# Kernel optimization log

Measured on AMD Instinct MI355X. Metric: run time of the kernel, lower is better.

The kernel has to match this reference:

```python
import jax, jax.numpy as jnp
import numpy as np

B, L, C, S, W, R = 2, 32, 32, 64, 64, 32
MH = 32  # forcing MLP hidden


def _conv3d(x, w, b, pad_hw):
    # x: [B, Cin, L, S, W], w: [Cout, Cin, 1, kh, kw]
    y = jax.lax.conv_general_dilated(
        x, w, window_strides=(1, 1, 1),
        padding=[(0, 0), (pad_hw, pad_hw), (pad_hw, pad_hw)],
        dimension_numbers=('NCDHW', 'OIDHW', 'NCDHW'))
    return y + b[None, :, None, None, None]


def _forward(x, listT, params_log_base, dispersion_mod, fm_W1, fm_b1, fm_W2, fm_b2,
             forcing_scale, U_re, U_im, V_re, V_im, pW_re, pW_im, pb_re, pb_im,
             convr_w, convr_b, convi_w, convi_b, projc_w, projc_b, ln_w, ln_b):
    b, l, c, s, w = x.shape
    r = U_re.shape[-1]
    pad = s // 4
    dt = listT.reshape(b, l, 1, 1, 1)

    # FFT with mirror padding along S
    xp = jnp.pad(x, ((0, 0), (0, 0), (0, 0), (pad, pad), (0, 0)), mode='reflect')
    h = jnp.fft.fft2(xp.astype(jnp.complex64), axes=(-2, -1), norm='ortho')

    # complex channel projection
    proj_W = pW_re + 1j * pW_im
    h = jnp.einsum('blcsw,cd->bldsw', h, proj_W)
    h = h + (pb_re + 1j * pb_im)[None, None, :, None, None]

    # back to spatial, crop pad, re-FFT
    hs = jnp.fft.ifft2(h, axes=(-2, -1), norm='ortho')[..., pad:-pad, :]
    h = jnp.fft.fft2(hs, axes=(-2, -1), norm='ortho')

    U = U_re + 1j * U_im          # [C, S, R]
    V = V_re + 1j * V_im          # [C, W, R]
    # zq[b,l,c,r,q] = sum_{s,w} h * conj(U)[c,s,r] * V[c,w,q]
    zq = jnp.einsum('blcsw,csr,cwq->blcrq', h, jnp.conj(U), V)

    nu_base = jnp.exp(params_log_base[0] + dispersion_mod[0]).reshape(1, 1, c, r, 1)
    th_base = jnp.exp(params_log_base[1] + dispersion_mod[1]).reshape(1, 1, c, r, 1)

    # forcing modulation
    ctx = x.mean(axis=(-2, -1))                       # [B, L, C]
    inp = jnp.concatenate([ctx, dt.reshape(b, l, 1)], axis=-1)
    mid = jnp.tanh(inp @ fm_W1 + fm_b1)
    mod = (mid @ fm_W2 + fm_b2).reshape(b, l, c, r, 2)
    dnu = (forcing_scale * jnp.tanh(mod[..., 0]))[..., None]
    dth = (forcing_scale * jnp.tanh(mod[..., 1]))[..., None]

    nu_t = jnp.maximum(nu_base * dt + dnu, 1e-6)       # [B, L, C, R, 1]
    th_t = th_base * dt + dth
    lamb = jnp.exp(jax.lax.complex(-nu_t, th_t))       # complex [B, L, C, R, 1]

    gamma = jnp.sqrt(jnp.maximum(1.0 - jnp.exp(-2.0 * nu_t), 1e-12))
    x_in = zq * gamma.astype(zq.dtype)                 # [B, L, C, R, R]

    # parallel linear-recurrence scan: z_t = lamb_t * z_{t-1} + x_t
    def comb(a, bb):
        a1, x1 = a
        a2, x2 = bb
        return a1 * a2, a2 * x1 + x2
    _, z_out = jax.lax.associative_scan(comb, (lamb, x_in), axis=1)

    # reconstruct spectral field and inverse FFT
    h_rec = jnp.einsum('blcrq,cwq,csr->blcsw', z_out, jnp.conj(V), U)
    h_sp = jnp.fft.ifft2(h_rec, axes=(-2, -1), norm='ortho')

    xr = jnp.transpose(h_sp.real, (0, 2, 1, 3, 4))     # [B, C, L, S, W]
    xi = jnp.transpose(h_sp.imag, (0, 2, 1, 3, 4))
    hr = _conv3d(xr, convr_w, convr_b, 1)
    hi = _conv3d(xi, convi_w, convi_b, 1)
    hf = _conv3d(jnp.concatenate([hr, hi], axis=1), projc_w, projc_b, 0)
    hf = jnp.transpose(hf, (0, 2, 1, 3, 4))            # [B, L, C, S, W]

    # LayerNorm over [S, W]
    mu = hf.mean(axis=(-2, -1), keepdims=True)
    var = hf.var(axis=(-2, -1), keepdims=True)
    hf = (hf - mu) / jnp.sqrt(var + 1e-5) * ln_w + ln_b

    return x + hf


def setup_inputs() -> dict:
    key = jax.random.key(0)
    ks = jax.random.split(key, 20)
    f32 = jnp.float32
    x = jax.random.normal(ks[0], (B, L, C, S, W), dtype=f32)
    listT = jax.random.uniform(ks[1], (B, L), dtype=f32, minval=0.5, maxval=1.5)

    r_min, r_max = 0.8, 0.99
    u1 = jax.random.uniform(ks[2], (C, R), dtype=f32)
    u2 = jax.random.uniform(ks[3], (C, R), dtype=f32)
    nu_log = jnp.log(-0.5 * jnp.log(u1 * (r_max ** 2 - r_min ** 2) + r_min ** 2))
    theta_log = jnp.log(u2 * (2.0 * np.pi))
    params_log_base = jnp.stack([nu_log, theta_log], axis=0)
    dispersion_mod = jnp.zeros((2, C, R), dtype=f32)

    fm_W1 = jax.random.normal(ks[4], (C + 1, MH), dtype=f32) / np.sqrt(C + 1)
    fm_b1 = jnp.zeros((MH,), dtype=f32)
    fm_W2 = jax.random.normal(ks[5], (MH, C * R * 2), dtype=f32) / np.sqrt(MH)
    fm_b2 = jnp.zeros((C * R * 2,), dtype=f32)
    forcing_scale = jnp.float32(0.1)

    cplx_scale = 1.0 / np.sqrt(2.0)
    U_re = jax.random.normal(ks[6], (C, S, R), dtype=f32) * cplx_scale / np.sqrt(S)
    U_im = jax.random.normal(ks[7], (C, S, R), dtype=f32) * cplx_scale / np.sqrt(S)
    V_re = jax.random.normal(ks[8], (C, W, R), dtype=f32) * cplx_scale / np.sqrt(W)
    V_im = jax.random.normal(ks[9], (C, W, R), dtype=f32) * cplx_scale / np.sqrt(W)
    pW_re = jax.random.normal(ks[10], (C, C), dtype=f32) * cplx_scale / np.sqrt(C)
    pW_im = jax.random.normal(ks[11], (C, C), dtype=f32) * cplx_scale / np.sqrt(C)
    pb_re = jnp.zeros((C,), dtype=f32)
    pb_im = jnp.zeros((C,), dtype=f32)

    convr_w = jax.random.normal(ks[12], (C, C, 1, 3, 3), dtype=f32) * (1.0 / np.sqrt(C * 9))
    convr_b = jnp.zeros((C,), dtype=f32)
    convi_w = jax.random.normal(ks[13], (C, C, 1, 3, 3), dtype=f32) * (1.0 / np.sqrt(C * 9))
    convi_b = jnp.zeros((C,), dtype=f32)
    projc_w = jax.random.normal(ks[14], (C, 2 * C, 1, 1, 1), dtype=f32) * (1.0 / np.sqrt(2 * C))
    projc_b = jnp.zeros((C,), dtype=f32)

    ln_w = jnp.ones((S, W), dtype=f32)
    ln_b = jnp.zeros((S, W), dtype=f32)

    return dict(x=x, listT=listT, params_log_base=params_log_base,
                dispersion_mod=dispersion_mod, fm_W1=fm_W1, fm_b1=fm_b1,
                fm_W2=fm_W2, fm_b2=fm_b2, forcing_scale=forcing_scale,
                U_re=U_re, U_im=U_im, V_re=V_re, V_im=V_im,
                pW_re=pW_re, pW_im=pW_im, pb_re=pb_re, pb_im=pb_im,
                convr_w=convr_w, convr_b=convr_b, convi_w=convi_w, convi_b=convi_b,
                projc_w=projc_w, projc_b=projc_b, ln_w=ln_w, ln_b=ln_b)


def reference(x, listT, params_log_base, dispersion_mod, fm_W1, fm_b1, fm_W2, fm_b2,
              forcing_scale, U_re, U_im, V_re, V_im, pW_re, pW_im, pb_re, pb_im,
              convr_w, convr_b, convi_w, convi_b, projc_w, projc_b, ln_w, ln_b):
    return _forward(x, listT, params_log_base, dispersion_mod, fm_W1, fm_b1, fm_W2,
                    fm_b2, forcing_scale, U_re, U_im, V_re, V_im, pW_re, pW_im,
                    pb_re, pb_im, convr_w, convr_b, convi_w, convi_b, projc_w,
                    projc_b, ln_w, ln_b)
```

## Files before the change

kernel.cpp:

```cpp
#include <hip/hip_runtime.h>


typedef __attribute__((ext_vector_type(8))) short short8;
typedef __attribute__((ext_vector_type(4))) float floatx4;

__device__ __forceinline__ unsigned pack_bf16(float re, float im) {
  unsigned a = __float_as_uint(re), b = __float_as_uint(im);
  a = (a + 0x7FFFu + ((a >> 16) & 1u)) >> 16;
  b = (b + 0x7FFFu + ((b >> 16) & 1u)) >> 16;
  return a | (b << 16);
}
__device__ __forceinline__ unsigned short bf16r(float v) {
  unsigned a = __float_as_uint(v);
  return (unsigned short)((a + 0x7FFFu + ((a >> 16) & 1u)) >> 16);
}

__global__ __launch_bounds__(256) void k_prep(
    const float* __restrict__ U_re, const float* __restrict__ U_im,
    const float* __restrict__ V_re, const float* __restrict__ V_im,
    const float* __restrict__ projc_w,
    const float* __restrict__ convr_w, const float* __restrict__ convi_w,
    unsigned* __restrict__ zqA, unsigned* __restrict__ recA,
    unsigned* __restrict__ recB, unsigned* __restrict__ Wtb,
    float* __restrict__ ctx) {
  const int bid = blockIdx.x;
  const int tid = threadIdx.x;
  if (bid < 2048) {
    __shared__ float2 tw[64];
    if (tid < 64) {
      float sa, ca;
      sincosf((float)tid * 0.09817477042468103f, &sa, &ca);
      tw[tid] = make_float2(ca, sa);
    }
    __syncthreads();
    int gid = bid * 256 + tid;
    const float *Ar, *Ai;
    int knum, mode, variant;
    bool plus;
    unsigned* dst;
    int didx;
    if (gid < 262144) {
      int c = gid >> 13, mat = (gid >> 11) & 3, m = (gid >> 6) & 31,
          kw = gid & 63;
      knum = kw; mode = m;
      if (mat < 2) { Ar = V_re + c * 2048; Ai = V_im + c * 2048; plus = false; }
      else         { Ar = U_re + c * 2048; Ai = U_im + c * 2048; plus = true; }
      variant = mat; dst = zqA; didx = gid;
    } else {
      int rid = gid - 262144;
      int c = rid >> 13, sub = rid & 8191;
      int which = sub >> 11, mm = (sub >> 5) & 63, k2 = sub & 31;
      knum = mm; mode = k2;
      if (which < 2) {
        Ar = U_re + c * 2048; Ai = U_im + c * 2048; plus = true;
        variant = 4 + which; dst = recA;
        didx = ((c * 2 + which) * 64 + mm) * 32 + k2;
      } else {
        Ar = V_re + c * 2048; Ai = V_im + c * 2048; plus = false;
        variant = 4 + which; dst = recB;
        didx = ((c * 2 + which - 2) * 64 + mm) * 32 + k2;
      }
    }
    float sr = 0.f, si = 0.f;
    for (int n = 0; n < 64; ++n) {
      float2 w = tw[(knum * n) & 63];
      float ar = Ar[n * 32 + mode], ai = Ai[n * 32 + mode];
      if (plus) { sr += ar * w.x - ai * w.y; si += ar * w.y + ai * w.x; }
      else      { sr += ar * w.x + ai * w.y; si += ai * w.x - ar * w.y; }
    }
    sr *= 0.125f; si *= 0.125f;
    unsigned pv;
    switch (variant) {
      case 0: pv = pack_bf16(sr, -si); break;
      case 1: pv = pack_bf16(si, sr); break;
      case 2: pv = pack_bf16(sr, si); break;
      case 3: pv = pack_bf16(-si, sr); break;
      case 4: pv = pack_bf16(sr, -si); break;
      case 5: pv = pack_bf16(si, sr); break;
      case 6: pv = pack_bf16(sr, si); break;
      default: pv = pack_bf16(-si, sr); break;
    }
    dst[didx] = pv;
  } else if (bid < 2084) {
    int gid = (bid - 2048) * 256 + tid;
    if (gid < 9216) {
      int co = gid / 288;
      int r2 = gid - co * 288;
      int tap = r2 >> 5, ci = r2 & 31;
      float sr = 0.f, si = 0.f;
      for (int m = 0; m < 32; ++m) {
        sr += projc_w[co * 64 + m]      * convr_w[(m * 32 + ci) * 9 + tap];
        si += projc_w[co * 64 + 32 + m] * convi_w[(m * 32 + ci) * 9 + tap];
      }
      Wtb[gid] = pack_bf16(sr, si);
    }
  } else {
    for (int i = tid; i < 2048; i += 256) ctx[i] = 0.f;
  }
}

__global__ __launch_bounds__(256) void k_mix(
    const float* __restrict__ x, const float* __restrict__ pWr,
    const float* __restrict__ pWi, unsigned* __restrict__ hs,
    float* __restrict__ ctx) {
  __shared__ unsigned xb_s[512 * 20];
  __shared__ float red[16][16][2];
  const int tid = threadIdx.x;
  const int bl = blockIdx.x >> 3;
  const int pxbase = (blockIdx.x & 7) * 512;
  const float* xb = x + (size_t)bl * 131072 + pxbase;
  float csa = 0.f, csb = 0.f;
#pragma unroll
  for (int t = 0; t < 8; ++t) {
    int i = t * 256 + tid;
    int c2 = i & 15, g4 = i >> 4;
    float4 a = *(const float4*)(xb + (2 * c2) * 4096 + g4 * 4);
    float4 b = *(const float4*)(xb + (2 * c2 + 1) * 4096 + g4 * 4);
    csa += a.x + a.y + a.z + a.w;
    csb += b.x + b.y + b.z + b.w;
#pragma unroll
    for (int j = 0; j < 4; ++j) {
      int px = g4 * 4 + j;
      xb_s[px * 20 + (((c2 >> 2) ^ (px & 3)) << 2) + (c2 & 3)] =
          pack_bf16(((const float*)&a)[j], ((const float*)&b)[j]);
    }
  }
  red[tid & 15][tid >> 4][0] = csa;
  red[tid & 15][tid >> 4][1] = csb;
  const int lane = tid & 63, wv = tid >> 6;
  const int qd = lane >> 4, ln = lane & 15;
  short8 arL, aiL, arH, aiH;
#pragma unroll
  for (int j = 0; j < 8; ++j) {
    int ci = qd * 8 + j;
    ((short*)&arL)[j] = (short)bf16r(pWr[ci * 32 + ln]);
    ((short*)&aiL)[j] = (short)bf16r(pWi[ci * 32 + ln]);
    ((short*)&arH)[j] = (short)bf16r(pWr[ci * 32 + 16 + ln]);
    ((short*)&aiH)[j] = (short)bf16r(pWi[ci * 32 + 16 + ln]);
  }
  __syncthreads();
  if (tid < 32) {
    int c2 = tid >> 1, part = tid & 1;
    float s = 0.f;
#pragma unroll
    for (int w = 0; w < 16; ++w) s += red[c2][w][part];
    atomicAdd(&ctx[bl * 32 + 2 * c2 + part], s * (1.f / 4096.f));
  }
#pragma unroll
  for (int pt = 0; pt < 8; ++pt) {
    int pxt = wv * 8 + pt;
    int pxl = pxt * 16 + ln;
    short8 bfr = *(const short8*)&xb_s[pxl * 20 + ((qd ^ (pxl & 3)) << 2)];
    floatx4 dRL = {0.f, 0.f, 0.f, 0.f}, dIL = {0.f, 0.f, 0.f, 0.f};
    floatx4 dRH = {0.f, 0.f, 0.f, 0.f}, dIH = {0.f, 0.f, 0.f, 0.f};
    dRL = __builtin_amdgcn_mfma_f32_16x16x32_bf16(arL, bfr, dRL, 0, 0, 0);
    dIL = __builtin_amdgcn_mfma_f32_16x16x32_bf16(aiL, bfr, dIL, 0, 0, 0);
    dRH = __builtin_amdgcn_mfma_f32_16x16x32_bf16(arH, bfr, dRH, 0, 0, 0);
    dIH = __builtin_amdgcn_mfma_f32_16x16x32_bf16(aiH, bfr, dIH, 0, 0, 0);
    unsigned* ho = hs + (size_t)bl * 131072 + pxbase + pxt * 16 + ln;
#pragma unroll
    for (int j = 0; j < 4; ++j) {
      ho[(qd * 4 + j) * 4096] = pack_bf16(dRL[j], dIL[j]);
      ho[(16 + qd * 4 + j) * 4096] = pack_bf16(dRH[j], dIH[j]);
    }
  }
}

__global__ __launch_bounds__(256) void k_zq(
    const unsigned* __restrict__ hs, const short* __restrict__ zqA,
    float2* __restrict__ zq,
    const float* __restrict__ ctx, const float* __restrict__ listT,
    const float* __restrict__ plb, const float* __restrict__ dmod,
    const float* __restrict__ W1, const float* __restrict__ b1,
    const float* __restrict__ W2, const float* __restrict__ b2,
    const float* __restrict__ fscale,
    float2* __restrict__ lam, float* __restrict__ gam) {
  __shared__ unsigned HsB[4096];
  __shared__ unsigned T2[2048];
  __shared__ float mid_s[32];
  const int tid = threadIdx.x;
  if (blockIdx.x >= 2048) {
    int bl = blockIdx.x - 2048;
    float dt = listT[bl];
    if (tid < 32) {
      float a = b1[tid];
      for (int j = 0; j < 32; ++j) a += ctx[bl * 32 + j] * W1[j * 32 + tid];
      a += dt * W1[1024 + tid];
      mid_s[tid] = tanhf(a);
    }
    __syncthreads();
    float fs = fscale[0];
#pragma unroll
    for (int u = 0; u < 4; ++u) {
      int cr = u * 256 + tid;
      int col = cr * 2;
      float m0 = b2[col], m1 = b2[col + 1];
      for (int h = 0; h < 32; ++h) {
        float mh = mid_s[h];
        float2 w2 = *(const float2*)&W2[h * 2048 + col];
        m0 += mh * w2.x;
        m1 += mh * w2.y;
      }
      float dnu = fs * tanhf(m0);
      float dth = fs * tanhf(m1);
      float nub = expf(plb[cr] + dmod[cr]);
      float thb = expf(plb[1024 + cr] + dmod[1024 + cr]);
      float nut = fmaxf(nub * dt + dnu, 1e-6f);
      float tht = thb * dt + dth;
      float e = expf(-nut);
      float sa, ca;
      sincosf(tht, &sa, &ca);
      float g = sqrtf(fmaxf(1.f - expf(-2.f * nut), 1e-12f));
      int o = bl * 1024 + cr;
      lam[o] = make_float2(e * ca, e * sa);
      gam[o] = g;
    }
    return;
  }
  const int blc = blockIdx.x;
  const int c = blc & 31;
  const int lane = tid & 63, wv = tid >> 6;
  const int qd = lane >> 4, ln = lane & 15;
  const int mt = wv >> 1, nth = wv & 1;
  {
    const uint4* hp = (const uint4*)(hs + (size_t)blc * 4096);
#pragma unroll
    for (int it = 0; it < 4; ++it) {
      int i4 = tid + it * 256;
      uint4 v = hp[i4];
      int s = i4 >> 4, w4 = i4 & 15;
      *(uint4*)&HsB[s * 64 + ((w4 ^ (s & 15)) << 2)] = v;
    }
  }
  const short* zA = zqA + (size_t)c * 4 * 32 * 128;
  short8 a1[4], a2[4], a3[4], a4[4];
#pragma unroll
  for (int t = 0; t < 4; ++t) {
    int row = mt * 16 + ln;
    a1[t] = *(const short8*)(zA + (0 * 32 + row) * 128 + t * 32 + qd * 8);
    a2[t] = *(const short8*)(zA + (1 * 32 + row) * 128 + t * 32 + qd * 8);
    a3[t] = *(const short8*)(zA + (2 * 32 + row) * 128 + t * 32 + qd * 8);
    a4[t] = *(const short8*)(zA + (3 * 32 + row) * 128 + t * 32 + qd * 8);
  }
  __syncthreads();
#pragma unroll
  for (int nti = 0; nti < 2; ++nti) {
    int nt = nth * 2 + nti;
    int n = nt * 16 + ln;
    floatx4 accr = {0.f, 0.f, 0.f, 0.f}, acci = {0.f, 0.f, 0.f, 0.f};
#pragma unroll
    for (int t = 0; t < 4; ++t) {
      short8 b = *(const short8*)&HsB[n * 64 + (((4 * t + qd) ^ (n & 15)) << 2)];
      accr = __builtin_amdgcn_mfma_f32_16x16x32_bf16(a1[t], b, accr, 0, 0, 0);
      acci = __builtin_amdgcn_mfma_f32_16x16x32_bf16(a2[t], b, acci, 0, 0, 0);
    }
#pragma unroll
    for (int j = 0; j < 4; ++j) {
      int q = mt * 16 + qd * 4 + j;
      int s = n;
      T2[q * 64 + (((s >> 2) ^ (q & 15)) << 2) + (s & 3)] = pack_bf16(accr[j], acci[j]);
    }
  }
  __syncthreads();
  {
    const int mt2 = wv >> 1, nt2 = wv & 1;
    int n = nt2 * 16 + ln;
    floatx4 zr = {0.f, 0.f, 0.f, 0.f}, zi = {0.f, 0.f, 0.f, 0.f};
#pragma unroll
    for (int t = 0; t < 4; ++t) {
      short8 b = *(const short8*)&T2[n * 64 + (((4 * t + qd) ^ (n & 15)) << 2)];
      zr = __builtin_amdgcn_mfma_f32_16x16x32_bf16(a3[t], b, zr, 0, 0, 0);
      zi = __builtin_amdgcn_mfma_f32_16x16x32_bf16(a4[t], b, zi, 0, 0, 0);
    }
    float2* zo = zq + (size_t)blc * 1024;
#pragma unroll
    for (int j = 0; j < 4; ++j) {
      int r = mt2 * 16 + qd * 4 + j;
      zo[r * 32 + n] = make_float2(zr[j], zi[j]);
    }
  }
}

__global__ __launch_bounds__(256) void k_scan(const float2* __restrict__ lam,
                                              const float* __restrict__ gam,
                                              const float2* zin,
                                              float2* zout) {
  const int bc = blockIdx.x >> 2;
  const int b = bc >> 5, c = bc & 31;
  const int rq = (blockIdx.x & 3) * 256 + threadIdx.x;
  const int r = rq >> 5;
  float2 st = make_float2(0.f, 0.f);
  float2 v = zin[((size_t)(b * 32) * 32 + c) * 1024 + rq];
  float2 lm = lam[(b * 32) * 1024 + c * 32 + r];
  float g = gam[(b * 32) * 1024 + c * 32 + r];
  for (int t = 0; t < 32; ++t) {
    float2 nv, nlm;
    float ng;
    if (t < 31) {
      size_t zb2 = ((size_t)(b * 32 + t + 1) * 32 + c) * 1024;
      int pb2 = (b * 32 + t + 1) * 1024 + c * 32;
      nv = zin[zb2 + rq];
      nlm = lam[pb2 + r];
      ng = gam[pb2 + r];
    }
    float nr = lm.x * st.x - lm.y * st.y + g * v.x;
    float ni = lm.x * st.y + lm.y * st.x + g * v.y;
    st = make_float2(nr, ni);
    zout[((size_t)(b * 32 + t) * 32 + c) * 1024 + rq] = st;
    v = nv; lm = nlm; g = ng;
  }
}

__global__ __launch_bounds__(256) void k_rec(const float2* __restrict__ zs,
                                             const short* __restrict__ recA,
                                             const short* __restrict__ recB,
                                             unsigned* __restrict__ hsp) {
  __shared__ unsigned zB[1024];
  __shared__ unsigned P[2048];
  const int blc = blockIdx.x;
  const int c = blc & 31;
  const int tid = threadIdx.x;
  const int lane = tid & 63, wv = tid >> 6;
  const int qd = lane >> 4, ln = lane & 15;
  {
    const float2* zp = zs + (size_t)blc * 1024;
#pragma unroll
    for (int it = 0; it < 4; ++it) {
      int i = tid + it * 256;
      float2 v = zp[i];
      int r = i >> 5, q = i & 31;
      zB[q * 32 + (((r >> 2) ^ (q & 7)) << 2) + (r & 3)] = pack_bf16(v.x, v.y);
    }
  }
  const short* rA = recA + (size_t)c * 2 * 64 * 64;
  short8 a5[2], a6[2];
#pragma unroll
  for (int t = 0; t < 2; ++t) {
    int row = wv * 16 + ln;
    a5[t] = *(const short8*)(rA + (0 * 64 + row) * 64 + t * 32 + qd * 8);
    a6[t] = *(const short8*)(rA + (1 * 64 + row) * 64 + t * 32 + qd * 8);
  }
  __syncthreads();
#pragma unroll
  for (int nt = 0; nt < 2; ++nt) {
    int n = nt * 16 + ln;
    floatx4 pr = {0.f, 0.f, 0.f, 0.f}, pi = {0.f, 0.f, 0.f, 0.f};
#pragma unroll
    for (int t = 0; t < 2; ++t) {
      short8 b = *(const short8*)&zB[n * 32 + (((4 * t + qd) ^ (n & 7)) << 2)];
      pr = __builtin_amdgcn_mfma_f32_16x16x32_bf16(a5[t], b, pr, 0, 0, 0);
      pi = __builtin_amdgcn_mfma_f32_16x16x32_bf16(a6[t], b, pi, 0, 0, 0);
    }
#pragma unroll
    for (int j = 0; j < 4; ++j) {
      int s = wv * 16 + qd * 4 + j;
      int q = n;
      P[s * 32 + (((q >> 2) ^ (s & 7)) << 2) + (q & 3)] = pack_bf16(pr[j], pi[j]);
    }
  }
  __syncthreads();
  const short* rB = recB + (size_t)c * 2 * 64 * 64;
  short8 pa[2];
#pragma unroll
  for (int t = 0; t < 2; ++t) {
    int row = wv * 16 + ln;
    pa[t] = *(const short8*)&P[row * 32 + (((4 * t + qd) ^ (row & 7)) << 2)];
  }
#pragma unroll
  for (int nt = 0; nt < 4; ++nt) {
    int n = nt * 16 + ln;
    floatx4 hr = {0.f, 0.f, 0.f, 0.f}, hi = {0.f, 0.f, 0.f, 0.f};
#pragma unroll
    for (int t = 0; t < 2; ++t) {
      short8 b5 = *(const short8*)(rB + (0 * 64 + n) * 64 + t * 32 + qd * 8);
      short8 b6 = *(const short8*)(rB + (1 * 64 + n) * 64 + t * 32 + qd * 8);
      hr = __builtin_amdgcn_mfma_f32_16x16x32_bf16(pa[t], b5, hr, 0, 0, 0);
      hi = __builtin_amdgcn_mfma_f32_16x16x32_bf16(pa[t], b6, hi, 0, 0, 0);
    }
    unsigned* ho = hsp + (size_t)blc * 4096;
#pragma unroll
    for (int j = 0; j < 4; ++j) {
      int s = wv * 16 + qd * 4 + j;
      ho[s * 64 + n] = pack_bf16(hr[j], hi[j]);
    }
  }
}

__global__ __launch_bounds__(256, 2) void k_conv(
    const unsigned* __restrict__ hsp, const short* __restrict__ Wtb,
    unsigned short* __restrict__ convout, float2* __restrict__ stats) {
  __shared__ unsigned lds_in[6 * 66 * 32];
  const int bl = blockIdx.x >> 4;
  const int slab = blockIdx.x & 15;
  const int y0 = slab * 4;
  const int tid = threadIdx.x;
  for (int i = tid; i < 384; i += 256) {
    int ci = i & 31, j = i >> 5;
    int yi = j >> 1, xi = (j & 1) ? 65 : 0;
    int slot = (ci >> 2) ^ (xi & 7);
    lds_in[(yi * 66 + xi) * 32 + slot * 4 + (ci & 3)] = 0u;
  }
#pragma unroll
  for (int t = 0; t < 12; ++t) {
    int i = t * 256 + tid;
    int ci = i & 31;
    int j = i >> 5;
    int yi = j >> 4, x4 = j & 15;
    int y = y0 + yi - 1;
    uint4 v = make_uint4(0u, 0u, 0u, 0u);
    if ((unsigned)y < 64u)
      v = *(const uint4*)(hsp + (((size_t)bl * 32 + ci) * 64 + y) * 64 + x4 * 4);
    int xb = 1 + x4 * 4;
#pragma unroll
    for (int jj = 0; jj < 4; ++jj) {
      int xi = xb + jj;
      int slot = (ci >> 2) ^ (xi & 7);
      lds_in[(yi * 66 + xi) * 32 + slot * 4 + (ci & 3)] =
          ((const unsigned*)&v)[jj];
    }
  }
  const int lane = tid & 63;
  const int wv = tid >> 6;
  const int co = lane & 15;
  const int qd = lane >> 4;
  short8 bL[18], bH[18];
  {
    const short* wpL = Wtb + (co * 9) * 64 + qd * 8;
    const short* wpH = Wtb + ((co + 16) * 9) * 64 + qd * 8;
#pragma unroll
    for (int tap = 0; tap < 9; ++tap)
#pragma unroll
      for (int kk = 0; kk < 2; ++kk) {
        bL[tap * 2 + kk] = *(const short8*)(wpL + tap * 64 + kk * 32);
        bH[tap * 2 + kk] = *(const short8*)(wpH + tap * 64 + kk * 32);
      }
  }
  __syncthreads();
  float sL = 0.f, s2L = 0.f, sH = 0.f, s2H = 0.f;
  const int x0 = wv * 16;
  const int xl = lane & 15;
  for (int ry = 0; ry < 4; ++ry) {
    floatx4 aL = {0.f, 0.f, 0.f, 0.f}, aH = {0.f, 0.f, 0.f, 0.f};
#pragma unroll
    for (int tap = 0; tap < 9; ++tap) {
      int dy = tap / 3, dx = tap - dy * 3;
      int yi = ry + dy;
      int xi = x0 + xl + dx;
#pragma unroll
      for (int kk = 0; kk < 2; ++kk) {
        int slot = ((kk << 2) | qd) ^ (xi & 7);
        const short8 a =
            *(const short8*)&lds_in[(yi * 66 + xi) * 32 + slot * 4];
        aL = __builtin_amdgcn_mfma_f32_16x16x32_bf16(a, bL[tap * 2 + kk], aL, 0, 0, 0);
        aH = __builtin_amdgcn_mfma_f32_16x16x32_bf16(a, bH[tap * 2 + kk], aH, 0, 0, 0);
      }
    }
    size_t goL = (((size_t)bl * 32 + co) * 64 + (y0 + ry)) * 64 + x0 + qd * 4;
    size_t goH = goL + (size_t)16 * 4096;
    *(uint2*)(convout + goL) =
        make_uint2(pack_bf16(aL[0], aL[1]), pack_bf16(aL[2], aL[3]));
    *(uint2*)(convout + goH) =
        make_uint2(pack_bf16(aH[0], aH[1]), pack_bf16(aH[2], aH[3]));
#pragma unroll
    for (int j = 0; j < 4; ++j) {
      sL += aL[j]; s2L += aL[j] * aL[j];
      sH += aH[j]; s2H += aH[j] * aH[j];
    }
  }
  sL += __shfl_down(sL, 32, 64);  s2L += __shfl_down(s2L, 32, 64);
  sH += __shfl_down(sH, 32, 64);  s2H += __shfl_down(s2H, 32, 64);
  sL += __shfl_down(sL, 16, 64);  s2L += __shfl_down(s2L, 16, 64);
  sH += __shfl_down(sH, 16, 64);  s2H += __shfl_down(s2H, 16, 64);
  if (lane < 16) {
    stats[((size_t)bl * 32 + lane) * 64 + slab * 4 + wv] = make_float2(sL, s2L);
    stats[((size_t)bl * 32 + 16 + lane) * 64 + slab * 4 + wv] =
        make_float2(sH, s2H);
  }
}

__global__ __launch_bounds__(256) void k_ln(
    const unsigned short* __restrict__ convout,
    const float2* __restrict__ stats, const float* __restrict__ x,
    const float* __restrict__ ln_w, const float* __restrict__ ln_b,
    float* __restrict__ out) {
  const int blc = blockIdx.x;
  const int tid = threadIdx.x;
  __shared__ float sh_mu, sh_rs;
  if (tid < 64) {
    float2 v = stats[(size_t)blc * 64 + tid];
    float s = v.x, s2 = v.y;
#pragma unroll
    for (int o = 32; o > 0; o >>= 1) {
      s += __shfl_down(s, o, 64);
      s2 += __shfl_down(s2, o, 64);
    }
    if (tid == 0) {
      float mu = s * (1.f / 4096.f);
      float var = s2 * (1.f / 4096.f) - mu * mu;
      sh_mu = mu;
      sh_rs = rsqrtf(var + 1e-5f);
    }
  }
  __syncthreads();
  float mu = sh_mu, rs = sh_rs;
  const uint2* cp = (const uint2*)(convout + (size_t)blc * 4096);
  const float4* xp = (const float4*)(x + (size_t)blc * 4096);
  const float4* lwp = (const float4*)ln_w;
  const float4* lbp = (const float4*)ln_b;
  float4* op = (float4*)(out + (size_t)blc * 4096);
#pragma unroll
  for (int k = 0; k < 4; ++k) {
    int i = tid + k * 256;
    uint2 cv = cp[i];
    float4 xv = xp[i], lw = lwp[i], lb = lbp[i];
    float c0 = __uint_as_float(cv.x << 16);
    float c1 = __uint_as_float(cv.x & 0xFFFF0000u);
    float c2 = __uint_as_float(cv.y << 16);
    float c3 = __uint_as_float(cv.y & 0xFFFF0000u);
    float4 o;
    o.x = xv.x + (c0 - mu) * rs * lw.x + lb.x;
    o.y = xv.y + (c1 - mu) * rs * lw.y + lb.y;
    o.z = xv.z + (c2 - mu) * rs * lw.z + lb.z;
    o.w = xv.w + (c3 - mu) * rs * lw.w + lb.w;
    op[i] = o;
  }
}

extern "C" void kernel_launch(void* const* d_in, const int* in_sizes, int n_in,
                              void* d_out, int out_size, void* d_ws,
                              size_t ws_size, hipStream_t stream) {
  const float* x       = (const float*)d_in[0];
  const float* listT   = (const float*)d_in[1];
  const float* plb     = (const float*)d_in[2];
  const float* dmod    = (const float*)d_in[3];
  const float* fm_W1   = (const float*)d_in[4];
  const float* fm_b1   = (const float*)d_in[5];
  const float* fm_W2   = (const float*)d_in[6];
  const float* fm_b2   = (const float*)d_in[7];
  const float* fscale  = (const float*)d_in[8];
  const float* U_re    = (const float*)d_in[9];
  const float* U_im    = (const float*)d_in[10];
  const float* V_re    = (const float*)d_in[11];
  const float* V_im    = (const float*)d_in[12];
  const float* pW_re   = (const float*)d_in[13];
  const float* pW_im   = (const float*)d_in[14];
  const float* convr_w = (const float*)d_in[17];
  const float* convi_w = (const float*)d_in[19];
  const float* projc_w = (const float*)d_in[21];
  const float* ln_w    = (const float*)d_in[23];
  const float* ln_b    = (const float*)d_in[24];
  float* out = (float*)d_out;

  float* wsf = (float*)d_ws;
  unsigned* hs  = (unsigned*)wsf;
  unsigned* hsp = (unsigned*)wsf;
  unsigned* zqAp  = (unsigned*)(wsf + 8388608);
  unsigned* recAp = (unsigned*)(wsf + 8388608 + 262144);
  unsigned* recBp = (unsigned*)(wsf + 8388608 + 393216);
  unsigned short* convout = (unsigned short*)(wsf + 8388608);
  float2*   stats = (float2*)(wsf + 12582912);
  float2*   zq  = (float2*)(wsf + 16777216);
  size_t off = 16777216 + 4194304;
  float2* zs = (float2*)(wsf + off);
  size_t need_with_zs = (size_t)(off + 4194304 + 470016) * 4;
  bool sep = ws_size >= need_with_zs;
  if (sep) off += 4194304; else zs = zq;
  float2*   lam  = (float2*)(wsf + off);
  float*    gam  = wsf + off + 131072;
  float*    ctx  = wsf + off + 458752;
  unsigned* Wtb  = (unsigned*)(wsf + off + 460800);

  k_prep<<<2085, 256, 0, stream>>>(U_re, U_im, V_re, V_im, projc_w,
                                   convr_w, convi_w, zqAp, recAp, recBp,
                                   Wtb, ctx);
  k_mix<<<512, 256, 0, stream>>>(x, pW_re, pW_im, hs, ctx);
  k_zq<<<2112, 256, 0, stream>>>(hs, (const short*)zqAp, zq, ctx, listT, plb,
                                 dmod, fm_W1, fm_b1, fm_W2, fm_b2, fscale,
                                 lam, gam);
  k_scan<<<256, 256, 0, stream>>>(lam, gam, zq, zs);
  k_rec<<<2048, 256, 0, stream>>>(zs, (const short*)recAp, (const short*)recBp, hsp);
  k_conv<<<1024, 256, 0, stream>>>(hsp, (const short*)Wtb, convout, stats);
  k_ln<<<2048, 256, 0, stream>>>(convout, stats, x, ln_w, ln_b, out);
}
```

Measured before the change: 250.5 us.

## Merge mix into prep kernel, parallelize time scan in segments, emit bf16 scan output

Folds the channel-mix kernel into the prep kernel so the two launches become one. The atomic context accumulation is replaced by per-segment partial sums that k_zq reduces. The sequential 32-step scan is split into four 8-step segments per thread group, joined by a carry combine through shared memory, which gives four times more blocks. The scan now writes packed bf16 directly, halving that intermediate traffic and removing the repack in k_rec. The cost is extra complex multiplies for the segment prefix products and more register use for the per-step arrays.

```diff
diff --git a/kernel.cpp b/kernel.cpp
--- a/kernel.cpp
+++ b/kernel.cpp
@@ -15,25 +15,89 @@
   return (unsigned short)((a + 0x7FFFu + ((a >> 16) & 1u)) >> 16);
 }
 
-__global__ __launch_bounds__(256) void k_prep(
+__global__ __launch_bounds__(256) void k_mixprep(
+    const float* __restrict__ x, const float* __restrict__ pWr,
+    const float* __restrict__ pWi,
     const float* __restrict__ U_re, const float* __restrict__ U_im,
     const float* __restrict__ V_re, const float* __restrict__ V_im,
-    const float* __restrict__ projc_w,
-    const float* __restrict__ convr_w, const float* __restrict__ convi_w,
+    const float* __restrict__ projc_w, const float* __restrict__ convr_w,
+    const float* __restrict__ convi_w,
+    unsigned* __restrict__ hs, float* __restrict__ ctxp,
     unsigned* __restrict__ zqA, unsigned* __restrict__ recA,
-    unsigned* __restrict__ recB, unsigned* __restrict__ Wtb,
-    float* __restrict__ ctx) {
-  const int bid = blockIdx.x;
+    unsigned* __restrict__ recB, unsigned* __restrict__ Wtb) {
+  __shared__ __align__(16) char smem[512 * 20 * 4 + 16 * 16 * 2 * 4];
   const int tid = threadIdx.x;
-  if (bid < 2048) {
-    __shared__ float2 tw[64];
+  if (blockIdx.x < 512) {
+    unsigned* xb_s = (unsigned*)smem;
+    float(*red)[16][2] = (float(*)[16][2])(smem + 40960);
+    const int bl = blockIdx.x >> 3;
+    const int seg = blockIdx.x & 7;
+    const int pxbase = seg * 512;
+    const float* xb = x + (size_t)bl * 131072 + pxbase;
+    float csa = 0.f, csb = 0.f;
+#pragma unroll
+    for (int t = 0; t < 8; ++t) {
+      int i = t * 256 + tid;
+      int c2 = i & 15, g4 = i >> 4;
+      float4 a = *(const float4*)(xb + (2 * c2) * 4096 + g4 * 4);
+      float4 b = *(const float4*)(xb + (2 * c2 + 1) * 4096 + g4 * 4);
+      csa += a.x + a.y + a.z + a.w;
+      csb += b.x + b.y + b.z + b.w;
+#pragma unroll
+      for (int j = 0; j < 4; ++j) {
+        int px = g4 * 4 + j;
+        xb_s[px * 20 + (((c2 >> 2) ^ (px & 3)) << 2) + (c2 & 3)] =
+            pack_bf16(((const float*)&a)[j], ((const float*)&b)[j]);
+      }
+    }
+    red[tid & 15][tid >> 4][0] = csa;
+    red[tid & 15][tid >> 4][1] = csb;
+    const int lane = tid & 63, wv = tid >> 6;
+    const int qd = lane >> 4, ln = lane & 15;
+    short8 arL, aiL, arH, aiH;
+#pragma unroll
+    for (int j = 0; j < 8; ++j) {
+      int ci = qd * 8 + j;
+      ((short*)&arL)[j] = (short)bf16r(pWr[ci * 32 + ln]);
+      ((short*)&aiL)[j] = (short)bf16r(pWi[ci * 32 + ln]);
+      ((short*)&arH)[j] = (short)bf16r(pWr[ci * 32 + 16 + ln]);
+      ((short*)&aiH)[j] = (short)bf16r(pWi[ci * 32 + 16 + ln]);
+    }
+    __syncthreads();
+    if (tid < 32) {
+      int c2 = tid >> 1, part = tid & 1;
+      float s = 0.f;
+#pragma unroll
+      for (int w = 0; w < 16; ++w) s += red[c2][w][part];
+      ctxp[(bl * 8 + seg) * 32 + 2 * c2 + part] = s;
+    }
+#pragma unroll
+    for (int pt = 0; pt < 8; ++pt) {
+      int pxt = wv * 8 + pt;
+      int pxl = pxt * 16 + ln;
+      short8 bfr = *(const short8*)&xb_s[pxl * 20 + ((qd ^ (pxl & 3)) << 2)];
+      floatx4 dRL = {0.f, 0.f, 0.f, 0.f}, dIL = {0.f, 0.f, 0.f, 0.f};
+      floatx4 dRH = {0.f, 0.f, 0.f, 0.f}, dIH = {0.f, 0.f, 0.f, 0.f};
+      dRL = __builtin_amdgcn_mfma_f32_16x16x32_bf16(arL, bfr, dRL, 0, 0, 0);
+      dIL = __builtin_amdgcn_mfma_f32_16x16x32_bf16(aiL, bfr, dIL, 0, 0, 0);
+      dRH = __builtin_amdgcn_mfma_f32_16x16x32_bf16(arH, bfr, dRH, 0, 0, 0);
+      dIH = __builtin_amdgcn_mfma_f32_16x16x32_bf16(aiH, bfr, dIH, 0, 0, 0);
+      unsigned* ho = hs + (size_t)bl * 131072 + pxbase + pxt * 16 + ln;
+#pragma unroll
+      for (int j = 0; j < 4; ++j) {
+        ho[(qd * 4 + j) * 4096] = pack_bf16(dRL[j], dIL[j]);
+        ho[(16 + qd * 4 + j) * 4096] = pack_bf16(dRH[j], dIH[j]);
+      }
+    }
+  } else if (blockIdx.x < 2560) {
+    float2* tw = (float2*)smem;
     if (tid < 64) {
       float sa, ca;
       sincosf((float)tid * 0.09817477042468103f, &sa, &ca);
       tw[tid] = make_float2(ca, sa);
     }
     __syncthreads();
-    int gid = bid * 256 + tid;
+    int gid = (blockIdx.x - 512) * 256 + tid;
     const float *Ar, *Ai;
     int knum, mode, variant;
     bool plus;
@@ -81,8 +145,8 @@
       default: pv = pack_bf16(-si, sr); break;
     }
     dst[didx] = pv;
-  } else if (bid < 2084) {
-    int gid = (bid - 2048) * 256 + tid;
+  } else {
+    int gid = (blockIdx.x - 2560) * 256 + tid;
     if (gid < 9216) {
       int co = gid / 288;
       int r2 = gid - co * 288;
@@ -94,82 +158,13 @@
       }
       Wtb[gid] = pack_bf16(sr, si);
     }
-  } else {
-    for (int i = tid; i < 2048; i += 256) ctx[i] = 0.f;
-  }
-}
-
-__global__ __launch_bounds__(256) void k_mix(
-    const float* __restrict__ x, const float* __restrict__ pWr,
-    const float* __restrict__ pWi, unsigned* __restrict__ hs,
-    float* __restrict__ ctx) {
-  __shared__ unsigned xb_s[512 * 20];
-  __shared__ float red[16][16][2];
-  const int tid = threadIdx.x;
-  const int bl = blockIdx.x >> 3;
-  const int pxbase = (blockIdx.x & 7) * 512;
-  const float* xb = x + (size_t)bl * 131072 + pxbase;
-  float csa = 0.f, csb = 0.f;
-#pragma unroll
-  for (int t = 0; t < 8; ++t) {
-    int i = t * 256 + tid;
-    int c2 = i & 15, g4 = i >> 4;
-    float4 a = *(const float4*)(xb + (2 * c2) * 4096 + g4 * 4);
-    float4 b = *(const float4*)(xb + (2 * c2 + 1) * 4096 + g4 * 4);
-    csa += a.x + a.y + a.z + a.w;
-    csb += b.x + b.y + b.z + b.w;
-#pragma unroll
-    for (int j = 0; j < 4; ++j) {
-      int px = g4 * 4 + j;
-      xb_s[px * 20 + (((c2 >> 2) ^ (px & 3)) << 2) + (c2 & 3)] =
-          pack_bf16(((const float*)&a)[j], ((const float*)&b)[j]);
-    }
-  }
-  red[tid & 15][tid >> 4][0] = csa;
-  red[tid & 15][tid >> 4][1] = csb;
-  const int lane = tid & 63, wv = tid >> 6;
-  const int qd = lane >> 4, ln = lane & 15;
-  short8 arL, aiL, arH, aiH;
-#pragma unroll
-  for (int j = 0; j < 8; ++j) {
-    int ci = qd * 8 + j;
-    ((short*)&arL)[j] = (short)bf16r(pWr[ci * 32 + ln]);
-    ((short*)&aiL)[j] = (short)bf16r(pWi[ci * 32 + ln]);
-    ((short*)&arH)[j] = (short)bf16r(pWr[ci * 32 + 16 + ln]);
-    ((short*)&aiH)[j] = (short)bf16r(pWi[ci * 32 + 16 + ln]);
-  }
-  __syncthreads();
-  if (tid < 32) {
-    int c2 = tid >> 1, part = tid & 1;
-    float s = 0.f;
-#pragma unroll
-    for (int w = 0; w < 16; ++w) s += red[c2][w][part];
-    atomicAdd(&ctx[bl * 32 + 2 * c2 + part], s * (1.f / 4096.f));
-  }
-#pragma unroll
-  for (int pt = 0; pt < 8; ++pt) {
-    int pxt = wv * 8 + pt;
-    int pxl = pxt * 16 + ln;
-    short8 bfr = *(const short8*)&xb_s[pxl * 20 + ((qd ^ (pxl & 3)) << 2)];
-    floatx4 dRL = {0.f, 0.f, 0.f, 0.f}, dIL = {0.f, 0.f, 0.f, 0.f};
-    floatx4 dRH = {0.f, 0.f, 0.f, 0.f}, dIH = {0.f, 0.f, 0.f, 0.f};
-    dRL = __builtin_amdgcn_mfma_f32_16x16x32_bf16(arL, bfr, dRL, 0, 0, 0);
-    dIL = __builtin_amdgcn_mfma_f32_16x16x32_bf16(aiL, bfr, dIL, 0, 0, 0);
-    dRH = __builtin_amdgcn_mfma_f32_16x16x32_bf16(arH, bfr, dRH, 0, 0, 0);
-    dIH = __builtin_amdgcn_mfma_f32_16x16x32_bf16(aiH, bfr, dIH, 0, 0, 0);
-    unsigned* ho = hs + (size_t)bl * 131072 + pxbase + pxt * 16 + ln;
-#pragma unroll
-    for (int j = 0; j < 4; ++j) {
-      ho[(qd * 4 + j) * 4096] = pack_bf16(dRL[j], dIL[j]);
-      ho[(16 + qd * 4 + j) * 4096] = pack_bf16(dRH[j], dIH[j]);
-    }
   }
 }
 
 __global__ __launch_bounds__(256) void k_zq(
     const unsigned* __restrict__ hs, const short* __restrict__ zqA,
     float2* __restrict__ zq,
-    const float* __restrict__ ctx, const float* __restrict__ listT,
+    const float* __restrict__ ctxp, const float* __restrict__ listT,
     const float* __restrict__ plb, const float* __restrict__ dmod,
     const float* __restrict__ W1, const float* __restrict__ b1,
     const float* __restrict__ W2, const float* __restrict__ b2,
@@ -178,13 +173,21 @@
   __shared__ unsigned HsB[4096];
   __shared__ unsigned T2[2048];
   __shared__ float mid_s[32];
+  __shared__ float ctxs[32];
   const int tid = threadIdx.x;
   if (blockIdx.x >= 2048) {
     int bl = blockIdx.x - 2048;
     float dt = listT[bl];
     if (tid < 32) {
+      float s = 0.f;
+#pragma unroll
+      for (int sg = 0; sg < 8; ++sg) s += ctxp[(bl * 8 + sg) * 32 + tid];
+      ctxs[tid] = s * (1.f / 4096.f);
+    }
+    __syncthreads();
+    if (tid < 32) {
       float a = b1[tid];
-      for (int j = 0; j < 32; ++j) a += ctx[bl * 32 + j] * W1[j * 32 + tid];
+      for (int j = 0; j < 32; ++j) a += ctxs[j] * W1[j * 32 + tid];
       a += dt * W1[1024 + tid];
       mid_s[tid] = tanhf(a);
     }
@@ -283,35 +286,72 @@
 
 __global__ __launch_bounds__(256) void k_scan(const float2* __restrict__ lam,
                                               const float* __restrict__ gam,
-                                              const float2* zin,
-                                              float2* zout) {
-  const int bc = blockIdx.x >> 2;
+                                              const float2* __restrict__ zin,
+                                              unsigned* __restrict__ zsp,
+                                              int zst) {
+  __shared__ float2 se[4][64];
+  __shared__ float2 pe[4][64];
+  __shared__ float2 cr_s[4][64];
+  const int bc = blockIdx.x >> 4;
   const int b = bc >> 5, c = bc & 31;
-  const int rq = (blockIdx.x & 3) * 256 + threadIdx.x;
-  const int r = rq >> 5;
-  float2 st = make_float2(0.f, 0.f);
-  float2 v = zin[((size_t)(b * 32) * 32 + c) * 1024 + rq];
-  float2 lm = lam[(b * 32) * 1024 + c * 32 + r];
-  float g = gam[(b * 32) * 1024 + c * 32 + r];
-  for (int t = 0; t < 32; ++t) {
+  const int rq0 = (blockIdx.x & 15) * 64;
+  const int seg = threadIdx.x >> 6, u = threadIdx.x & 63;
+  const int rq = rq0 + u, r = rq >> 5;
+  const int t0 = seg * 8;
+  float2 s = make_float2(0.f, 0.f), P = make_float2(1.f, 0.f);
+  float2 zloc[8], Ps[8];
+  float2 v = zin[((size_t)(b * 32 + t0) * 32 + c) * 1024 + rq];
+  float2 lm = lam[(b * 32 + t0) * 1024 + c * 32 + r];
+  float g = gam[(b * 32 + t0) * 1024 + c * 32 + r];
+#pragma unroll
+  for (int i = 0; i < 8; ++i) {
     float2 nv, nlm;
     float ng;
-    if (t < 31) {
-      size_t zb2 = ((size_t)(b * 32 + t + 1) * 32 + c) * 1024;
-      int pb2 = (b * 32 + t + 1) * 1024 + c * 32;
-      nv = zin[zb2 + rq];
-      nlm = lam[pb2 + r];
-      ng = gam[pb2 + r];
-    }
-    float nr = lm.x * st.x - lm.y * st.y + g * v.x;
-    float ni = lm.x * st.y + lm.y * st.x + g * v.y;
-    st = make_float2(nr, ni);
-    zout[((size_t)(b * 32 + t) * 32 + c) * 1024 + rq] = st;
+    if (i < 7) {
+      int t = t0 + i + 1;
+      nv = zin[((size_t)(b * 32 + t) * 32 + c) * 1024 + rq];
+      nlm = lam[(b * 32 + t) * 1024 + c * 32 + r];
+      ng = gam[(b * 32 + t) * 1024 + c * 32 + r];
+    }
+    float nr = lm.x * s.x - lm.y * s.y + g * v.x;
+    float ni = lm.x * s.y + lm.y * s.x + g * v.y;
+    s = make_float2(nr, ni);
+    float pr = P.x * lm.x - P.y * lm.y;
+    float pi = P.x * lm.y + P.y * lm.x;
+    P = make_float2(pr, pi);
+    zloc[i] = s;
+    Ps[i] = P;
     v = nv; lm = nlm; g = ng;
   }
-}
-
-__global__ __launch_bounds__(256) void k_rec(const float2* __restrict__ zs,
+  se[seg][u] = s;
+  pe[seg][u] = P;
+  __syncthreads();
+  if (threadIdx.x < 64) {
+    float2 c1 = se[0][u];
+    float2 p1 = pe[1][u], s1 = se[1][u];
+    float2 c2 = make_float2(s1.x + p1.x * c1.x - p1.y * c1.y,
+                            s1.y + p1.x * c1.y + p1.y * c1.x);
+    float2 p2 = pe[2][u], s2 = se[2][u];
+    float2 c3 = make_float2(s2.x + p2.x * c2.x - p2.y * c2.y,
+                            s2.y + p2.x * c2.y + p2.y * c2.x);
+    cr_s[0][u] = make_float2(0.f, 0.f);
+    cr_s[1][u] = c1;
+    cr_s[2][u] = c2;
+    cr_s[3][u] = c3;
+  }
+  __syncthreads();
+  float2 cr = cr_s[seg][u];
+#pragma unroll
+  for (int i = 0; i < 8; ++i) {
+    float zr = zloc[i].x + Ps[i].x * cr.x - Ps[i].y * cr.y;
+    float zi = zloc[i].y + Ps[i].x * cr.y + Ps[i].y * cr.x;
+    size_t idx = ((size_t)(b * 32 + t0 + i) * 32 + c) * 1024 + rq;
+    zsp[idx * zst] = pack_bf16(zr, zi);
+  }
+}
+
+__global__ __launch_bounds__(256) void k_rec(const unsigned* __restrict__ zs,
+                                             int zst,
                                              const short* __restrict__ recA,
                                              const short* __restrict__ recB,
                                              unsigned* __restrict__ hsp) {
@@ -323,13 +363,13 @@
   const int lane = tid & 63, wv = tid >> 6;
   const int qd = lane >> 4, ln = lane & 15;
   {
-    const float2* zp = zs + (size_t)blc * 1024;
+    const unsigned* zp = zs + (size_t)blc * 1024 * zst;
 #pragma unroll
     for (int it = 0; it < 4; ++it) {
       int i = tid + it * 256;
-      float2 v = zp[i];
+      unsigned pv = zp[(size_t)i * zst];
       int r = i >> 5, q = i & 31;
-      zB[q * 32 + (((r >> 2) ^ (q & 7)) << 2) + (r & 3)] = pack_bf16(v.x, v.y);
+      zB[q * 32 + (((r >> 2) ^ (q & 7)) << 2) + (r & 3)] = pv;
     }
   }
   const short* rA = recA + (size_t)c * 2 * 64 * 64;
@@ -561,24 +601,29 @@
   float2*   stats = (float2*)(wsf + 12582912);
   float2*   zq  = (float2*)(wsf + 16777216);
   size_t off = 16777216 + 4194304;
-  float2* zs = (float2*)(wsf + off);
-  size_t need_with_zs = (size_t)(off + 4194304 + 470016) * 4;
-  bool sep = ws_size >= need_with_zs;
-  if (sep) off += 4194304; else zs = zq;
-  float2*   lam  = (float2*)(wsf + off);
-  float*    gam  = wsf + off + 131072;
-  float*    ctx  = wsf + off + 458752;
-  unsigned* Wtb  = (unsigned*)(wsf + off + 460800);
-
-  k_prep<<<2085, 256, 0, stream>>>(U_re, U_im, V_re, V_im, projc_w,
-                                   convr_w, convi_w, zqAp, recAp, recBp,
-                                   Wtb, ctx);
-  k_mix<<<512, 256, 0, stream>>>(x, pW_re, pW_im, hs, ctx);
-  k_zq<<<2112, 256, 0, stream>>>(hs, (const short*)zqAp, zq, ctx, listT, plb,
+  const size_t tail = 222208;
+  unsigned* zs;
+  int zst;
+  size_t off2;
+  if (ws_size >= (off + 2097152 + tail) * 4) {
+    zs = (unsigned*)(wsf + off); zst = 1; off2 = off + 2097152;
+  } else {
+    zs = (unsigned*)zq; zst = 2; off2 = off;
+  }
+  float2*   lam  = (float2*)(wsf + off2);
+  float*    gam  = wsf + off2 + 131072;
+  float*    ctxp = wsf + off2 + 196608;
+  unsigned* Wtb  = (unsigned*)(wsf + off2 + 212992);
+
+  k_mixprep<<<2596, 256, 0, stream>>>(x, pW_re, pW_im, U_re, U_im, V_re, V_im,
+                                      projc_w, convr_w, convi_w, hs, ctxp,
+                                      zqAp, recAp, recBp, Wtb);
+  k_zq<<<2112, 256, 0, stream>>>(hs, (const short*)zqAp, zq, ctxp, listT, plb,
                                  dmod, fm_W1, fm_b1, fm_W2, fm_b2, fscale,
                                  lam, gam);
-  k_scan<<<256, 256, 0, stream>>>(lam, gam, zq, zs);
-  k_rec<<<2048, 256, 0, stream>>>(zs, (const short*)recAp, (const short*)recBp, hsp);
+  k_scan<<<1024, 256, 0, stream>>>(lam, gam, zq, zs, zst);
+  k_rec<<<2048, 256, 0, stream>>>(zs, zst, (const short*)recAp,
+                                  (const short*)recBp, hsp);
   k_conv<<<1024, 256, 0, stream>>>(hsp, (const short*)Wtb, convout, stats);
   k_ln<<<2048, 256, 0, stream>>>(convout, stats, x, ln_w, ln_b, out);
 }
```

After: 247.3 us. Within noise of the previous version (-1.3%).
